# Kernel optimization log

Measured on AMD Instinct MI355X. Metric: run time of the kernel, lower is better.

The kernel has to match this reference:

```python
import jax, jax.numpy as jnp
import numpy as np

N_NODES = 50000
N_EDGES = 800000
D_IN = 64   # input_dimension + 1
D_HID = 64


def _gcn_conv(x, src, dst, W, b, deg_isqrt):
    # PyG GCNConv: X' = D^{-1/2} (A + I) D^{-1/2} X W + b
    h = x @ W  # [N, H]
    norm = (deg_isqrt[src] * deg_isqrt[dst])[:, None]  # [E, 1]
    agg = jax.ops.segment_sum(h[src] * norm, dst, num_segments=x.shape[0])
    # self-loop contribution: norm_ii = deg_isqrt[i]^2
    agg = agg + h * (deg_isqrt * deg_isqrt)[:, None]
    return agg + b


def setup_inputs() -> dict:
    key = jax.random.key(0)
    ks = jax.random.split(key, 8)
    x = jax.random.normal(ks[0], (N_NODES, D_IN), dtype=jnp.float32)
    edge_index = jax.random.randint(ks[1], (2, N_EDGES), 0, N_NODES, dtype=jnp.int32)
    s = 1.0 / np.sqrt(D_HID)
    W0 = jax.random.normal(ks[2], (D_IN, D_HID), dtype=jnp.float32) * s
    b0 = jnp.zeros((D_HID,), dtype=jnp.float32)
    W1 = jax.random.normal(ks[3], (D_HID, D_HID), dtype=jnp.float32) * s
    b1 = jnp.zeros((D_HID,), dtype=jnp.float32)
    W2 = jax.random.normal(ks[4], (D_HID, D_HID), dtype=jnp.float32) * s
    b2 = jnp.zeros((D_HID,), dtype=jnp.float32)
    Wout = jax.random.normal(ks[5], (D_HID, 1), dtype=jnp.float32) * s
    bout = jnp.zeros((1,), dtype=jnp.float32)
    return {"x": x, "edge_index": edge_index, "W0": W0, "b0": b0,
            "W1": W1, "b1": b1, "W2": W2, "b2": b2,
            "Wout": Wout, "bout": bout}


def reference(x, edge_index, W0, b0, W1, b1, W2, b2, Wout, bout):
    src, dst = edge_index[0], edge_index[1]
    n = x.shape[0]
    # degree with self-loop (edge weight 1.0 each)
    deg = jnp.zeros((n,), x.dtype).at[dst].add(1.0) + 1.0
    deg_isqrt = jax.lax.rsqrt(deg)
    h = jax.nn.relu(_gcn_conv(x, src, dst, W0, b0, deg_isqrt))
    h = jax.nn.relu(_gcn_conv(h, src, dst, W1, b1, deg_isqrt))
    h = jax.nn.relu(_gcn_conv(h, src, dst, W2, b2, deg_isqrt))
    return h @ Wout + bout  # [N, 1]
```

## Files before the change

### kernel.cpp

```cpp
#include <hip/hip_runtime.h>
#include <hip/hip_bf16.h>

#define D 64
#define N_NODES 50000
#define N_EDGES 800000
#define TILE 16

__global__ void hist_k(const int* __restrict__ dst, int* __restrict__ cnt, int E) {
    int i = blockIdx.x * blockDim.x + threadIdx.x;
    if (i < E) atomicAdd(&cnt[dst[i]], 1);
}

__global__ void scan1_k(const int* __restrict__ cnt, int* __restrict__ off,
                        int* __restrict__ bsum, float* __restrict__ dis, int N) {
    __shared__ int sh[256];
    int t = threadIdx.x;
    int i = blockIdx.x * 256 + t;
    int v = (i < N) ? cnt[i] : 0;
    sh[t] = v;
    __syncthreads();
#pragma unroll
    for (int d = 1; d < 256; d <<= 1) {
        int u = (t >= d) ? sh[t - d] : 0;
        __syncthreads();
        sh[t] += u;
        __syncthreads();
    }
    if (i < N) {
        off[i] = sh[t] - v;
        dis[i] = rsqrtf((float)v + 1.0f);
    }
    if (t == 255) bsum[blockIdx.x] = sh[255];
}

__global__ void scan2_k(int* __restrict__ bsum, int nb) {
    __shared__ int sh[256];
    int t = threadIdx.x;
    int v = (t < nb) ? bsum[t] : 0;
    sh[t] = v;
    __syncthreads();
#pragma unroll
    for (int d = 1; d < 256; d <<= 1) {
        int u = (t >= d) ? sh[t - d] : 0;
        __syncthreads();
        sh[t] += u;
        __syncthreads();
    }
    if (t < nb) bsum[t] = sh[t] - v;
}

__global__ void scan3_k(int* __restrict__ off, const int* __restrict__ bsum,
                        int* __restrict__ cursor, int N, int E) {
    int i = blockIdx.x * 256 + threadIdx.x;
    if (i < N) {
        int o = off[i] + bsum[blockIdx.x];
        off[i] = o;
        cursor[i] = o;
    }
    if (i == 0) off[N] = E;
}

__device__ __forceinline__ void fma4(float4& a, float s, float4 w) {
    a.x = fmaf(s, w.x, a.x);
    a.y = fmaf(s, w.y, a.y);
    a.z = fmaf(s, w.z, a.z);
    a.w = fmaf(s, w.w, a.w);
}

template <int SCALED>
__device__ __forceinline__ void tile_gemm(const float (*hbuf)[68], const float4* __restrict__ W4,
                                          const float* __restrict__ dis, float* __restrict__ outp,
                                          int base, int t) {
    int lane = t & 63;
    int cg = lane & 15;
    int rr = (t >> 6) * 4 + (lane >> 4);
    float4 acc = make_float4(0.f, 0.f, 0.f, 0.f);
#pragma unroll
    for (int kk = 0; kk < 16; ++kk) {
        float4 hb = *(const float4*)&hbuf[rr][kk * 4];
        fma4(acc, hb.x, W4[(kk * 4 + 0) * 16 + cg]);
        fma4(acc, hb.y, W4[(kk * 4 + 1) * 16 + cg]);
        fma4(acc, hb.z, W4[(kk * 4 + 2) * 16 + cg]);
        fma4(acc, hb.w, W4[(kk * 4 + 3) * 16 + cg]);
    }
    if (SCALED) {
        float dv = dis[base + rr];
        acc.x *= dv; acc.y *= dv; acc.z *= dv; acc.w *= dv;
    }
    ((float4*)outp)[(size_t)(base + rr) * 16 + cg] = acc;
}

__global__ void gemm0_k(const float4* __restrict__ X4, const float4* __restrict__ W4,
                        float* __restrict__ H, int N) {
    __shared__ float hbuf[TILE][68];
    int t = threadIdx.x;
    int base = blockIdx.x * TILE;
    int r = t >> 4, ch = t & 15;
    float4 v = X4[(size_t)(base + r) * 16 + ch];
    *(float4*)&hbuf[r][ch * 4] = v;
    __syncthreads();
    tile_gemm<0>(hbuf, W4, nullptr, H, base, t);
}

__global__ void fused_fill_k(const int* __restrict__ src, const int* __restrict__ dst,
                             int* __restrict__ cursor, int* __restrict__ esrc,
                             float4* __restrict__ H4, const float* __restrict__ dis,
                             int N, int E, int fillBlocks) {
    int bid = blockIdx.x;
    int t = threadIdx.x;
    if (bid < fillBlocks) {
        for (int i = bid * 256 + t; i < E; i += fillBlocks * 256) {
            int pos = atomicAdd(&cursor[dst[i]], 1);
            esrc[pos] = src[i];
        }
    } else {
        int sb = bid - fillBlocks;
        int nsb = gridDim.x - fillBlocks;
        int total = N * 16;
        for (int i = sb * 256 + t; i < total; i += nsb * 256) {
            float4 v = H4[i];
            float dv = dis[i >> 4];
            v.x *= dv; v.y *= dv; v.z *= dv; v.w *= dv;
            H4[i] = v;
        }
    }
}

template <int FINAL>
__global__ void layer_k(const float4* __restrict__ Hs4, const int* __restrict__ off,
                        const int* __restrict__ esrc, const float* __restrict__ dis,
                        const float* __restrict__ bias, const float4* __restrict__ W4,
                        const float* __restrict__ bout, float* __restrict__ outp, int N) {
    __shared__ float hbuf[TILE][68];
    int t = threadIdx.x;
    int lane = t & 63;
    int w = t >> 6;
    int g = lane >> 4;
    int l16 = lane & 15;
    int rloc = w * 4 + g;
    int n = blockIdx.x * TILE + rloc;

    int beg = off[n], end = off[n + 1];
    float4 acc = Hs4[(size_t)n * 16 + l16];
    int j = beg;
    for (; j + 8 <= end; j += 8) {
        int s0 = esrc[j],     s1 = esrc[j + 1], s2 = esrc[j + 2], s3 = esrc[j + 3];
        int s4 = esrc[j + 4], s5 = esrc[j + 5], s6 = esrc[j + 6], s7 = esrc[j + 7];
        float4 v0 = Hs4[(size_t)s0 * 16 + l16];
        float4 v1 = Hs4[(size_t)s1 * 16 + l16];
        float4 v2 = Hs4[(size_t)s2 * 16 + l16];
        float4 v3 = Hs4[(size_t)s3 * 16 + l16];
        float4 v4 = Hs4[(size_t)s4 * 16 + l16];
        float4 v5 = Hs4[(size_t)s5 * 16 + l16];
        float4 v6 = Hs4[(size_t)s6 * 16 + l16];
        float4 v7 = Hs4[(size_t)s7 * 16 + l16];
        acc.x += ((v0.x + v1.x) + (v2.x + v3.x)) + ((v4.x + v5.x) + (v6.x + v7.x));
        acc.y += ((v0.y + v1.y) + (v2.y + v3.y)) + ((v4.y + v5.y) + (v6.y + v7.y));
        acc.z += ((v0.z + v1.z) + (v2.z + v3.z)) + ((v4.z + v5.z) + (v6.z + v7.z));
        acc.w += ((v0.w + v1.w) + (v2.w + v3.w)) + ((v4.w + v5.w) + (v6.w + v7.w));
    }
    if (j < end) {
        int last = end - 1;
        int i1 = j + 1 <= last ? j + 1 : last;
        int i2 = j + 2 <= last ? j + 2 : last;
        int i3 = j + 3 <= last ? j + 3 : last;
        int i4 = j + 4 <= last ? j + 4 : last;
        int i5 = j + 5 <= last ? j + 5 : last;
        int i6 = j + 6 <= last ? j + 6 : last;
        int i7 = j + 7 <= last ? j + 7 : last;
        int s0 = esrc[j],  s1 = esrc[i1], s2 = esrc[i2], s3 = esrc[i3];
        int s4 = esrc[i4], s5 = esrc[i5], s6 = esrc[i6], s7 = esrc[i7];
        float m1 = (j + 1 < end) ? 1.f : 0.f;
        float m2 = (j + 2 < end) ? 1.f : 0.f;
        float m3 = (j + 3 < end) ? 1.f : 0.f;
        float m4 = (j + 4 < end) ? 1.f : 0.f;
        float m5 = (j + 5 < end) ? 1.f : 0.f;
        float m6 = (j + 6 < end) ? 1.f : 0.f;
        float m7 = (j + 7 < end) ? 1.f : 0.f;
        float4 v0 = Hs4[(size_t)s0 * 16 + l16];
        float4 v1 = Hs4[(size_t)s1 * 16 + l16];
        float4 v2 = Hs4[(size_t)s2 * 16 + l16];
        float4 v3 = Hs4[(size_t)s3 * 16 + l16];
        float4 v4 = Hs4[(size_t)s4 * 16 + l16];
        float4 v5 = Hs4[(size_t)s5 * 16 + l16];
        float4 v6 = Hs4[(size_t)s6 * 16 + l16];
        float4 v7 = Hs4[(size_t)s7 * 16 + l16];
        acc.x += v0.x;           acc.y += v0.y;           acc.z += v0.z;           acc.w += v0.w;
        acc.x = fmaf(m1, v1.x, acc.x); acc.y = fmaf(m1, v1.y, acc.y); acc.z = fmaf(m1, v1.z, acc.z); acc.w = fmaf(m1, v1.w, acc.w);
        acc.x = fmaf(m2, v2.x, acc.x); acc.y = fmaf(m2, v2.y, acc.y); acc.z = fmaf(m2, v2.z, acc.z); acc.w = fmaf(m2, v2.w, acc.w);
        acc.x = fmaf(m3, v3.x, acc.x); acc.y = fmaf(m3, v3.y, acc.y); acc.z = fmaf(m3, v3.z, acc.z); acc.w = fmaf(m3, v3.w, acc.w);
        acc.x = fmaf(m4, v4.x, acc.x); acc.y = fmaf(m4, v4.y, acc.y); acc.z = fmaf(m4, v4.z, acc.z); acc.w = fmaf(m4, v4.w, acc.w);
        acc.x = fmaf(m5, v5.x, acc.x); acc.y = fmaf(m5, v5.y, acc.y); acc.z = fmaf(m5, v5.z, acc.z); acc.w = fmaf(m5, v5.w, acc.w);
        acc.x = fmaf(m6, v6.x, acc.x); acc.y = fmaf(m6, v6.y, acc.y); acc.z = fmaf(m6, v6.z, acc.z); acc.w = fmaf(m6, v6.w, acc.w);
        acc.x = fmaf(m7, v7.x, acc.x); acc.y = fmaf(m7, v7.y, acc.y); acc.z = fmaf(m7, v7.z, acc.z); acc.w = fmaf(m7, v7.w, acc.w);
    }

    float dv = dis[n];
    float4 b4 = ((const float4*)bias)[l16];
    float4 h4;
    h4.x = fmaxf(fmaf(acc.x, dv, b4.x), 0.f);
    h4.y = fmaxf(fmaf(acc.y, dv, b4.y), 0.f);
    h4.z = fmaxf(fmaf(acc.z, dv, b4.z), 0.f);
    h4.w = fmaxf(fmaf(acc.w, dv, b4.w), 0.f);

    if (FINAL) {
        float4 w4 = ((const float4*)W4)[l16];
        float p = fmaf(h4.x, w4.x, fmaf(h4.y, w4.y, fmaf(h4.z, w4.z, h4.w * w4.w)));
        p += __shfl_xor(p, 1, 64);
        p += __shfl_xor(p, 2, 64);
        p += __shfl_xor(p, 4, 64);
        p += __shfl_xor(p, 8, 64);
        if (l16 == 0) outp[n] = p + bout[0];
    } else {
        *(float4*)&hbuf[rloc][l16 * 4] = h4;
        __syncthreads();
        tile_gemm<1>(hbuf, W4, dis, outp, blockIdx.x * TILE, t);
    }
}

extern "C" void kernel_launch(void* const* d_in, const int* in_sizes, int n_in,
                              void* d_out, int out_size, void* d_ws, size_t ws_size,
                              hipStream_t stream) {
    const float* x    = (const float*)d_in[0];
    const int*   ei   = (const int*)d_in[1];
    const float* W0   = (const float*)d_in[2];
    const float* b0   = (const float*)d_in[3];
    const float* W1   = (const float*)d_in[4];
    const float* b1   = (const float*)d_in[5];
    const float* W2   = (const float*)d_in[6];
    const float* b2   = (const float*)d_in[7];
    const float* Wout = (const float*)d_in[8];
    const float* bout = (const float*)d_in[9];
    float* out = (float*)d_out;

    const int N = N_NODES, E = N_EDGES;
    const int* src = ei;
    const int* dst = ei + E;

    char* ws = (char*)d_ws;
    int*   cnt    = (int*)(ws);
    int*   off    = (int*)(ws + (256u << 10));
    int*   cursor = (int*)(ws + (512u << 10));
    float* dis    = (float*)(ws + (768u << 10));
    int*   bsum   = (int*)(ws + (990u << 10));
    int*   esrc   = (int*)(ws + (1u << 20));
    float* bufA   = (float*)(ws + (5u << 20));
    float* bufB   = (float*)(ws + (18u << 20));

    dim3 blk(256);
    const int NB = (N + 255) / 256;
    dim3 gN(NB);
    dim3 gE((E + 255) / 256);
    const int TILES = N / TILE;
    dim3 gTile(TILES);
    const int FILL_BLOCKS = 3125;
    const int SCALE_BLOCKS = 784;

    hipMemsetAsync(cnt, 0, (size_t)N * sizeof(int), stream);
    hist_k<<<gE, blk, 0, stream>>>(dst, cnt, E);
    gemm0_k<<<gTile, blk, 0, stream>>>((const float4*)x, (const float4*)W0, bufA, N);

    scan1_k<<<gN, blk, 0, stream>>>(cnt, off, bsum, dis, N);
    scan2_k<<<1, blk, 0, stream>>>(bsum, NB);
    scan3_k<<<gN, blk, 0, stream>>>(off, bsum, cursor, N, E);

    fused_fill_k<<<dim3(FILL_BLOCKS + SCALE_BLOCKS), blk, 0, stream>>>(
        src, dst, cursor, esrc, (float4*)bufA, dis, N, E, FILL_BLOCKS);

    layer_k<0><<<gTile, blk, 0, stream>>>((const float4*)bufA, off, esrc, dis,
                                          b0, (const float4*)W1, nullptr, bufB, N);
    layer_k<0><<<gTile, blk, 0, stream>>>((const float4*)bufB, off, esrc, dis,
                                          b1, (const float4*)W2, nullptr, bufA, N);
    layer_k<1><<<gTile, blk, 0, stream>>>((const float4*)bufA, off, esrc, dis,
                                          b2, (const float4*)Wout, bout, out, N);
}
```

Before: 307.4 us.

## Fuse scan with first GEMM, merge scan stages, process two nodes per thread group

Merges the first scan pass with the initial dense GEMM into one launch and folds the block-sum scan into the final scan kernel, where every block rescans the block sums itself. This removes two kernel launches. The layer kernels now handle 32 nodes per block, with each 16-lane group aggregating two nodes in an interleaved loop so more independent gathers are in flight, and the tile GEMM reuses each loaded weight for two rows. In exchange the grid is halved, which may lower occupancy, and load imbalance between the paired nodes' degrees can leave lanes idle.

```diff
diff --git a/kernel.cpp b/kernel.cpp
--- a/kernel.cpp
+++ b/kernel.cpp
@@ -4,36 +4,96 @@
 #define D 64
 #define N_NODES 50000
 #define N_EDGES 800000
-#define TILE 16
+#define TILE 32
+#define SCAN_BLKS 196
 
 __global__ void hist_k(const int* __restrict__ dst, int* __restrict__ cnt, int E) {
     int i = blockIdx.x * blockDim.x + threadIdx.x;
     if (i < E) atomicAdd(&cnt[dst[i]], 1);
 }
 
-__global__ void scan1_k(const int* __restrict__ cnt, int* __restrict__ off,
-                        int* __restrict__ bsum, float* __restrict__ dis, int N) {
-    __shared__ int sh[256];
+__device__ __forceinline__ void fma4(float4& a, float s, float4 w) {
+    a.x = fmaf(s, w.x, a.x);
+    a.y = fmaf(s, w.y, a.y);
+    a.z = fmaf(s, w.z, a.z);
+    a.w = fmaf(s, w.w, a.w);
+}
+
+template <int SCALED>
+__device__ __forceinline__ void tile_gemm32(const float (*hbuf)[68], const float4* __restrict__ W4,
+                                            const float* __restrict__ dis, float* __restrict__ outp,
+                                            int base, int t, int N) {
+    int lane = t & 63;
+    int cg = lane & 15;
+    int rr = (t >> 6) * 4 + (lane >> 4);
+    int r1 = rr + 16;
+    float4 a0 = make_float4(0.f, 0.f, 0.f, 0.f);
+    float4 a1 = make_float4(0.f, 0.f, 0.f, 0.f);
+#pragma unroll
+    for (int kk = 0; kk < 16; ++kk) {
+        float4 h0 = *(const float4*)&hbuf[rr][kk * 4];
+        float4 h1 = *(const float4*)&hbuf[r1][kk * 4];
+        float4 w0 = W4[(kk * 4 + 0) * 16 + cg];
+        float4 w1 = W4[(kk * 4 + 1) * 16 + cg];
+        float4 w2 = W4[(kk * 4 + 2) * 16 + cg];
+        float4 w3 = W4[(kk * 4 + 3) * 16 + cg];
+        fma4(a0, h0.x, w0); fma4(a0, h0.y, w1); fma4(a0, h0.z, w2); fma4(a0, h0.w, w3);
+        fma4(a1, h1.x, w0); fma4(a1, h1.y, w1); fma4(a1, h1.z, w2); fma4(a1, h1.w, w3);
+    }
+    if (SCALED) {
+        float d0 = dis[base + rr];
+        a0.x *= d0; a0.y *= d0; a0.z *= d0; a0.w *= d0;
+    }
+    ((float4*)outp)[(size_t)(base + rr) * 16 + cg] = a0;
+    if (base + r1 < N) {
+        if (SCALED) {
+            float d1 = dis[base + r1];
+            a1.x *= d1; a1.y *= d1; a1.z *= d1; a1.w *= d1;
+        }
+        ((float4*)outp)[(size_t)(base + r1) * 16 + cg] = a1;
+    }
+}
+
+__global__ void scan1_gemm0_k(const int* __restrict__ cnt, int* __restrict__ off,
+                              int* __restrict__ bsum, float* __restrict__ dis,
+                              const float4* __restrict__ X4, const float4* __restrict__ W4,
+                              float* __restrict__ H, int N, int scanBlocks) {
+    __shared__ float hbuf[TILE][68];
+    int bid = blockIdx.x;
     int t = threadIdx.x;
-    int i = blockIdx.x * 256 + t;
-    int v = (i < N) ? cnt[i] : 0;
-    sh[t] = v;
-    __syncthreads();
+    if (bid < scanBlocks) {
+        int* sh = (int*)hbuf;
+        int i = bid * 256 + t;
+        int v = (i < N) ? cnt[i] : 0;
+        sh[t] = v;
+        __syncthreads();
 #pragma unroll
-    for (int d = 1; d < 256; d <<= 1) {
-        int u = (t >= d) ? sh[t - d] : 0;
-        __syncthreads();
-        sh[t] += u;
-        __syncthreads();
-    }
-    if (i < N) {
-        off[i] = sh[t] - v;
-        dis[i] = rsqrtf((float)v + 1.0f);
-    }
-    if (t == 255) bsum[blockIdx.x] = sh[255];
-}
-
-__global__ void scan2_k(int* __restrict__ bsum, int nb) {
+        for (int d = 1; d < 256; d <<= 1) {
+            int u = (t >= d) ? sh[t - d] : 0;
+            __syncthreads();
+            sh[t] += u;
+            __syncthreads();
+        }
+        if (i < N) {
+            off[i] = sh[t] - v;
+            dis[i] = rsqrtf((float)v + 1.0f);
+        }
+        if (t == 255) bsum[bid] = sh[255];
+    } else {
+        int base = (bid - scanBlocks) * TILE;
+        for (int idx = t; idx < TILE * 16; idx += 256) {
+            int r = idx >> 4, ch = idx & 15;
+            float4 v = (base + r < N) ? X4[(size_t)(base + r) * 16 + ch]
+                                      : make_float4(0.f, 0.f, 0.f, 0.f);
+            *(float4*)&hbuf[r][ch * 4] = v;
+        }
+        __syncthreads();
+        tile_gemm32<0>(hbuf, W4, nullptr, H, base, t, N);
+    }
+}
+
+__global__ void scan3_k(int* __restrict__ off, const int* __restrict__ bsum,
+                        int* __restrict__ cursor, int N, int E, int nb) {
     __shared__ int sh[256];
     int t = threadIdx.x;
     int v = (t < nb) ? bsum[t] : 0;
@@ -46,60 +106,14 @@
         sh[t] += u;
         __syncthreads();
     }
-    if (t < nb) bsum[t] = sh[t] - v;
-}
-
-__global__ void scan3_k(int* __restrict__ off, const int* __restrict__ bsum,
-                        int* __restrict__ cursor, int N, int E) {
-    int i = blockIdx.x * 256 + threadIdx.x;
+    int add = (blockIdx.x == 0) ? 0 : sh[blockIdx.x - 1];
+    int i = blockIdx.x * 256 + t;
     if (i < N) {
-        int o = off[i] + bsum[blockIdx.x];
+        int o = off[i] + add;
         off[i] = o;
         cursor[i] = o;
     }
     if (i == 0) off[N] = E;
-}
-
-__device__ __forceinline__ void fma4(float4& a, float s, float4 w) {
-    a.x = fmaf(s, w.x, a.x);
-    a.y = fmaf(s, w.y, a.y);
-    a.z = fmaf(s, w.z, a.z);
-    a.w = fmaf(s, w.w, a.w);
-}
-
-template <int SCALED>
-__device__ __forceinline__ void tile_gemm(const float (*hbuf)[68], const float4* __restrict__ W4,
-                                          const float* __restrict__ dis, float* __restrict__ outp,
-                                          int base, int t) {
-    int lane = t & 63;
-    int cg = lane & 15;
-    int rr = (t >> 6) * 4 + (lane >> 4);
-    float4 acc = make_float4(0.f, 0.f, 0.f, 0.f);
-#pragma unroll
-    for (int kk = 0; kk < 16; ++kk) {
-        float4 hb = *(const float4*)&hbuf[rr][kk * 4];
-        fma4(acc, hb.x, W4[(kk * 4 + 0) * 16 + cg]);
-        fma4(acc, hb.y, W4[(kk * 4 + 1) * 16 + cg]);
-        fma4(acc, hb.z, W4[(kk * 4 + 2) * 16 + cg]);
-        fma4(acc, hb.w, W4[(kk * 4 + 3) * 16 + cg]);
-    }
-    if (SCALED) {
-        float dv = dis[base + rr];
-        acc.x *= dv; acc.y *= dv; acc.z *= dv; acc.w *= dv;
-    }
-    ((float4*)outp)[(size_t)(base + rr) * 16 + cg] = acc;
-}
-
-__global__ void gemm0_k(const float4* __restrict__ X4, const float4* __restrict__ W4,
-                        float* __restrict__ H, int N) {
-    __shared__ float hbuf[TILE][68];
-    int t = threadIdx.x;
-    int base = blockIdx.x * TILE;
-    int r = t >> 4, ch = t & 15;
-    float4 v = X4[(size_t)(base + r) * 16 + ch];
-    *(float4*)&hbuf[r][ch * 4] = v;
-    __syncthreads();
-    tile_gemm<0>(hbuf, W4, nullptr, H, base, t);
 }
 
 __global__ void fused_fill_k(const int* __restrict__ src, const int* __restrict__ dst,
@@ -126,95 +140,132 @@
     }
 }
 
+__device__ __forceinline__ void batch8(const float4* __restrict__ Hs4,
+                                       const int* __restrict__ esrc,
+                                       int j, int l16, float4& acc) {
+    int s0 = esrc[j],     s1 = esrc[j + 1], s2 = esrc[j + 2], s3 = esrc[j + 3];
+    int s4 = esrc[j + 4], s5 = esrc[j + 5], s6 = esrc[j + 6], s7 = esrc[j + 7];
+    float4 v0 = Hs4[(size_t)s0 * 16 + l16];
+    float4 v1 = Hs4[(size_t)s1 * 16 + l16];
+    float4 v2 = Hs4[(size_t)s2 * 16 + l16];
+    float4 v3 = Hs4[(size_t)s3 * 16 + l16];
+    float4 v4 = Hs4[(size_t)s4 * 16 + l16];
+    float4 v5 = Hs4[(size_t)s5 * 16 + l16];
+    float4 v6 = Hs4[(size_t)s6 * 16 + l16];
+    float4 v7 = Hs4[(size_t)s7 * 16 + l16];
+    acc.x += ((v0.x + v1.x) + (v2.x + v3.x)) + ((v4.x + v5.x) + (v6.x + v7.x));
+    acc.y += ((v0.y + v1.y) + (v2.y + v3.y)) + ((v4.y + v5.y) + (v6.y + v7.y));
+    acc.z += ((v0.z + v1.z) + (v2.z + v3.z)) + ((v4.z + v5.z) + (v6.z + v7.z));
+    acc.w += ((v0.w + v1.w) + (v2.w + v3.w)) + ((v4.w + v5.w) + (v6.w + v7.w));
+}
+
+__device__ __forceinline__ void tail8(const float4* __restrict__ Hs4,
+                                      const int* __restrict__ esrc,
+                                      int j, int end, int l16, float4& acc) {
+    if (j >= end) return;
+    int last = end - 1;
+    int i1 = j + 1 <= last ? j + 1 : last;
+    int i2 = j + 2 <= last ? j + 2 : last;
+    int i3 = j + 3 <= last ? j + 3 : last;
+    int i4 = j + 4 <= last ? j + 4 : last;
+    int i5 = j + 5 <= last ? j + 5 : last;
+    int i6 = j + 6 <= last ? j + 6 : last;
+    int i7 = j + 7 <= last ? j + 7 : last;
+    int s0 = esrc[j],  s1 = esrc[i1], s2 = esrc[i2], s3 = esrc[i3];
+    int s4 = esrc[i4], s5 = esrc[i5], s6 = esrc[i6], s7 = esrc[i7];
+    float m1 = (j + 1 < end) ? 1.f : 0.f;
+    float m2 = (j + 2 < end) ? 1.f : 0.f;
+    float m3 = (j + 3 < end) ? 1.f : 0.f;
+    float m4 = (j + 4 < end) ? 1.f : 0.f;
+    float m5 = (j + 5 < end) ? 1.f : 0.f;
+    float m6 = (j + 6 < end) ? 1.f : 0.f;
+    float m7 = (j + 7 < end) ? 1.f : 0.f;
+    float4 v0 = Hs4[(size_t)s0 * 16 + l16];
+    float4 v1 = Hs4[(size_t)s1 * 16 + l16];
+    float4 v2 = Hs4[(size_t)s2 * 16 + l16];
+    float4 v3 = Hs4[(size_t)s3 * 16 + l16];
+    float4 v4 = Hs4[(size_t)s4 * 16 + l16];
+    float4 v5 = Hs4[(size_t)s5 * 16 + l16];
+    float4 v6 = Hs4[(size_t)s6 * 16 + l16];
+    float4 v7 = Hs4[(size_t)s7 * 16 + l16];
+    acc.x += v0.x; acc.y += v0.y; acc.z += v0.z; acc.w += v0.w;
+    acc.x = fmaf(m1, v1.x, acc.x); acc.y = fmaf(m1, v1.y, acc.y); acc.z = fmaf(m1, v1.z, acc.z); acc.w = fmaf(m1, v1.w, acc.w);
+    acc.x = fmaf(m2, v2.x, acc.x); acc.y = fmaf(m2, v2.y, acc.y); acc.z = fmaf(m2, v2.z, acc.z); acc.w = fmaf(m2, v2.w, acc.w);
+    acc.x = fmaf(m3, v3.x, acc.x); acc.y = fmaf(m3, v3.y, acc.y); acc.z = fmaf(m3, v3.z, acc.z); acc.w = fmaf(m3, v3.w, acc.w);
+    acc.x = fmaf(m4, v4.x, acc.x); acc.y = fmaf(m4, v4.y, acc.y); acc.z = fmaf(m4, v4.z, acc.z); acc.w = fmaf(m4, v4.w, acc.w);
+    acc.x = fmaf(m5, v5.x, acc.x); acc.y = fmaf(m5, v5.y, acc.y); acc.z = fmaf(m5, v5.z, acc.z); acc.w = fmaf(m5, v5.w, acc.w);
+    acc.x = fmaf(m6, v6.x, acc.x); acc.y = fmaf(m6, v6.y, acc.y); acc.z = fmaf(m6, v6.z, acc.z); acc.w = fmaf(m6, v6.w, acc.w);
+    acc.x = fmaf(m7, v7.x, acc.x); acc.y = fmaf(m7, v7.y, acc.y); acc.z = fmaf(m7, v7.z, acc.z); acc.w = fmaf(m7, v7.w, acc.w);
+}
+
 template <int FINAL>
 __global__ void layer_k(const float4* __restrict__ Hs4, const int* __restrict__ off,
                         const int* __restrict__ esrc, const float* __restrict__ dis,
                         const float* __restrict__ bias, const float4* __restrict__ W4,
                         const float* __restrict__ bout, float* __restrict__ outp, int N) {
-    __shared__ float hbuf[TILE][68];
     int t = threadIdx.x;
     int lane = t & 63;
     int w = t >> 6;
     int g = lane >> 4;
     int l16 = lane & 15;
     int rloc = w * 4 + g;
-    int n = blockIdx.x * TILE + rloc;
-
-    int beg = off[n], end = off[n + 1];
-    float4 acc = Hs4[(size_t)n * 16 + l16];
-    int j = beg;
-    for (; j + 8 <= end; j += 8) {
-        int s0 = esrc[j],     s1 = esrc[j + 1], s2 = esrc[j + 2], s3 = esrc[j + 3];
-        int s4 = esrc[j + 4], s5 = esrc[j + 5], s6 = esrc[j + 6], s7 = esrc[j + 7];
-        float4 v0 = Hs4[(size_t)s0 * 16 + l16];
-        float4 v1 = Hs4[(size_t)s1 * 16 + l16];
-        float4 v2 = Hs4[(size_t)s2 * 16 + l16];
-        float4 v3 = Hs4[(size_t)s3 * 16 + l16];
-        float4 v4 = Hs4[(size_t)s4 * 16 + l16];
-        float4 v5 = Hs4[(size_t)s5 * 16 + l16];
-        float4 v6 = Hs4[(size_t)s6 * 16 + l16];
-        float4 v7 = Hs4[(size_t)s7 * 16 + l16];
-        acc.x += ((v0.x + v1.x) + (v2.x + v3.x)) + ((v4.x + v5.x) + (v6.x + v7.x));
-        acc.y += ((v0.y + v1.y) + (v2.y + v3.y)) + ((v4.y + v5.y) + (v6.y + v7.y));
-        acc.z += ((v0.z + v1.z) + (v2.z + v3.z)) + ((v4.z + v5.z) + (v6.z + v7.z));
-        acc.w += ((v0.w + v1.w) + (v2.w + v3.w)) + ((v4.w + v5.w) + (v6.w + v7.w));
-    }
-    if (j < end) {
-        int last = end - 1;
-        int i1 = j + 1 <= last ? j + 1 : last;
-        int i2 = j + 2 <= last ? j + 2 : last;
-        int i3 = j + 3 <= last ? j + 3 : last;
-        int i4 = j + 4 <= last ? j + 4 : last;
-        int i5 = j + 5 <= last ? j + 5 : last;
-        int i6 = j + 6 <= last ? j + 6 : last;
-        int i7 = j + 7 <= last ? j + 7 : last;
-        int s0 = esrc[j],  s1 = esrc[i1], s2 = esrc[i2], s3 = esrc[i3];
-        int s4 = esrc[i4], s5 = esrc[i5], s6 = esrc[i6], s7 = esrc[i7];
-        float m1 = (j + 1 < end) ? 1.f : 0.f;
-        float m2 = (j + 2 < end) ? 1.f : 0.f;
-        float m3 = (j + 3 < end) ? 1.f : 0.f;
-        float m4 = (j + 4 < end) ? 1.f : 0.f;
-        float m5 = (j + 5 < end) ? 1.f : 0.f;
-        float m6 = (j + 6 < end) ? 1.f : 0.f;
-        float m7 = (j + 7 < end) ? 1.f : 0.f;
-        float4 v0 = Hs4[(size_t)s0 * 16 + l16];
-        float4 v1 = Hs4[(size_t)s1 * 16 + l16];
-        float4 v2 = Hs4[(size_t)s2 * 16 + l16];
-        float4 v3 = Hs4[(size_t)s3 * 16 + l16];
-        float4 v4 = Hs4[(size_t)s4 * 16 + l16];
-        float4 v5 = Hs4[(size_t)s5 * 16 + l16];
-        float4 v6 = Hs4[(size_t)s6 * 16 + l16];
-        float4 v7 = Hs4[(size_t)s7 * 16 + l16];
-        acc.x += v0.x;           acc.y += v0.y;           acc.z += v0.z;           acc.w += v0.w;
-        acc.x = fmaf(m1, v1.x, acc.x); acc.y = fmaf(m1, v1.y, acc.y); acc.z = fmaf(m1, v1.z, acc.z); acc.w = fmaf(m1, v1.w, acc.w);
-        acc.x = fmaf(m2, v2.x, acc.x); acc.y = fmaf(m2, v2.y, acc.y); acc.z = fmaf(m2, v2.z, acc.z); acc.w = fmaf(m2, v2.w, acc.w);
-        acc.x = fmaf(m3, v3.x, acc.x); acc.y = fmaf(m3, v3.y, acc.y); acc.z = fmaf(m3, v3.z, acc.z); acc.w = fmaf(m3, v3.w, acc.w);
-        acc.x = fmaf(m4, v4.x, acc.x); acc.y = fmaf(m4, v4.y, acc.y); acc.z = fmaf(m4, v4.z, acc.z); acc.w = fmaf(m4, v4.w, acc.w);
-        acc.x = fmaf(m5, v5.x, acc.x); acc.y = fmaf(m5, v5.y, acc.y); acc.z = fmaf(m5, v5.z, acc.z); acc.w = fmaf(m5, v5.w, acc.w);
-        acc.x = fmaf(m6, v6.x, acc.x); acc.y = fmaf(m6, v6.y, acc.y); acc.z = fmaf(m6, v6.z, acc.z); acc.w = fmaf(m6, v6.w, acc.w);
-        acc.x = fmaf(m7, v7.x, acc.x); acc.y = fmaf(m7, v7.y, acc.y); acc.z = fmaf(m7, v7.z, acc.z); acc.w = fmaf(m7, v7.w, acc.w);
-    }
-
-    float dv = dis[n];
+    int base = blockIdx.x * TILE;
+    int nA = base + rloc;
+    int nB = nA + 16;
+    bool vB = (nB < N);
+
+    int begA = off[nA], endA = off[nA + 1];
+    float4 accA = Hs4[(size_t)nA * 16 + l16];
+    int begB = 0, endB = 0;
+    float4 accB = make_float4(0.f, 0.f, 0.f, 0.f);
+    if (vB) {
+        begB = off[nB]; endB = off[nB + 1];
+        accB = Hs4[(size_t)nB * 16 + l16];
+    }
+
+    int jA = begA, jB = begB;
+    while (jA + 8 <= endA && jB + 8 <= endB) {
+        batch8(Hs4, esrc, jA, l16, accA);
+        batch8(Hs4, esrc, jB, l16, accB);
+        jA += 8; jB += 8;
+    }
+    while (jA + 8 <= endA) { batch8(Hs4, esrc, jA, l16, accA); jA += 8; }
+    while (jB + 8 <= endB) { batch8(Hs4, esrc, jB, l16, accB); jB += 8; }
+    tail8(Hs4, esrc, jA, endA, l16, accA);
+    tail8(Hs4, esrc, jB, endB, l16, accB);
+
+    float dvA = dis[nA];
+    float dvB = vB ? dis[nB] : 0.f;
     float4 b4 = ((const float4*)bias)[l16];
-    float4 h4;
-    h4.x = fmaxf(fmaf(acc.x, dv, b4.x), 0.f);
-    h4.y = fmaxf(fmaf(acc.y, dv, b4.y), 0.f);
-    h4.z = fmaxf(fmaf(acc.z, dv, b4.z), 0.f);
-    h4.w = fmaxf(fmaf(acc.w, dv, b4.w), 0.f);
+    float4 hA, hB;
+    hA.x = fmaxf(fmaf(accA.x, dvA, b4.x), 0.f);
+    hA.y = fmaxf(fmaf(accA.y, dvA, b4.y), 0.f);
+    hA.z = fmaxf(fmaf(accA.z, dvA, b4.z), 0.f);
+    hA.w = fmaxf(fmaf(accA.w, dvA, b4.w), 0.f);
+    hB.x = fmaxf(fmaf(accB.x, dvB, b4.x), 0.f);
+    hB.y = fmaxf(fmaf(accB.y, dvB, b4.y), 0.f);
+    hB.z = fmaxf(fmaf(accB.z, dvB, b4.z), 0.f);
+    hB.w = fmaxf(fmaf(accB.w, dvB, b4.w), 0.f);
 
     if (FINAL) {
         float4 w4 = ((const float4*)W4)[l16];
-        float p = fmaf(h4.x, w4.x, fmaf(h4.y, w4.y, fmaf(h4.z, w4.z, h4.w * w4.w)));
-        p += __shfl_xor(p, 1, 64);
-        p += __shfl_xor(p, 2, 64);
-        p += __shfl_xor(p, 4, 64);
-        p += __shfl_xor(p, 8, 64);
-        if (l16 == 0) outp[n] = p + bout[0];
+        float pA = fmaf(hA.x, w4.x, fmaf(hA.y, w4.y, fmaf(hA.z, w4.z, hA.w * w4.w)));
+        float pB = fmaf(hB.x, w4.x, fmaf(hB.y, w4.y, fmaf(hB.z, w4.z, hB.w * w4.w)));
+        pA += __shfl_xor(pA, 1, 64);  pB += __shfl_xor(pB, 1, 64);
+        pA += __shfl_xor(pA, 2, 64);  pB += __shfl_xor(pB, 2, 64);
+        pA += __shfl_xor(pA, 4, 64);  pB += __shfl_xor(pB, 4, 64);
+        pA += __shfl_xor(pA, 8, 64);  pB += __shfl_xor(pB, 8, 64);
+        if (l16 == 0) {
+            float b = bout[0];
+            outp[nA] = pA + b;
+            if (vB) outp[nB] = pB + b;
+        }
     } else {
-        *(float4*)&hbuf[rloc][l16 * 4] = h4;
-        __syncthreads();
-        tile_gemm<1>(hbuf, W4, dis, outp, blockIdx.x * TILE, t);
+        __shared__ float hbuf[TILE][68];
+        *(float4*)&hbuf[rloc][l16 * 4] = hA;
+        *(float4*)&hbuf[rloc + 16][l16 * 4] = hB;
+        __syncthreads();
+        tile_gemm32<1>(hbuf, W4, dis, outp, base, t, N);
     }
 }
 
@@ -248,21 +299,19 @@
     float* bufB   = (float*)(ws + (18u << 20));
 
     dim3 blk(256);
-    const int NB = (N + 255) / 256;
-    dim3 gN(NB);
     dim3 gE((E + 255) / 256);
-    const int TILES = N / TILE;
+    const int TILES = (N + TILE - 1) / TILE;
     dim3 gTile(TILES);
     const int FILL_BLOCKS = 3125;
     const int SCALE_BLOCKS = 784;
 
     hipMemsetAsync(cnt, 0, (size_t)N * sizeof(int), stream);
     hist_k<<<gE, blk, 0, stream>>>(dst, cnt, E);
-    gemm0_k<<<gTile, blk, 0, stream>>>((const float4*)x, (const float4*)W0, bufA, N);
-
-    scan1_k<<<gN, blk, 0, stream>>>(cnt, off, bsum, dis, N);
-    scan2_k<<<1, blk, 0, stream>>>(bsum, NB);
-    scan3_k<<<gN, blk, 0, stream>>>(off, bsum, cursor, N, E);
+
+    scan1_gemm0_k<<<dim3(SCAN_BLKS + TILES), blk, 0, stream>>>(
+        cnt, off, bsum, dis, (const float4*)x, (const float4*)W0, bufA, N, SCAN_BLKS);
+
+    scan3_k<<<dim3(SCAN_BLKS), blk, 0, stream>>>(off, bsum, cursor, N, E, SCAN_BLKS);
 
     fused_fill_k<<<dim3(FILL_BLOCKS + SCALE_BLOCKS), blk, 0, stream>>>(
         src, dst, cursor, esrc, (float4*)bufA, dis, N, E, FILL_BLOCKS);
```

After: 553.8 us. 80.2% more time.

## Fuse scan phase one with first GEMM and fold block-sum scan into scan3

Applied to the files above, without the earlier changes.

Merges the first scan pass and the layer-0 feature GEMM into one heterogeneous launch, where some blocks scan degree counts and the rest compute X@W0. The GEMM now works on 32-row tiles so each W load serves two rows. The separate block-sum scan kernel is removed; every scan3 block rescans the 196 block sums itself. Together this removes two kernel launches and their serialization gaps. The cost is redundant scan work in each scan3 block and more register pressure in the GEMM path.

```diff
diff --git a/kernel.cpp b/kernel.cpp
--- a/kernel.cpp
+++ b/kernel.cpp
@@ -5,59 +5,12 @@
 #define N_NODES 50000
 #define N_EDGES 800000
 #define TILE 16
+#define GTILE 32
+#define SCAN_BLKS 196
 
 __global__ void hist_k(const int* __restrict__ dst, int* __restrict__ cnt, int E) {
     int i = blockIdx.x * blockDim.x + threadIdx.x;
     if (i < E) atomicAdd(&cnt[dst[i]], 1);
-}
-
-__global__ void scan1_k(const int* __restrict__ cnt, int* __restrict__ off,
-                        int* __restrict__ bsum, float* __restrict__ dis, int N) {
-    __shared__ int sh[256];
-    int t = threadIdx.x;
-    int i = blockIdx.x * 256 + t;
-    int v = (i < N) ? cnt[i] : 0;
-    sh[t] = v;
-    __syncthreads();
-#pragma unroll
-    for (int d = 1; d < 256; d <<= 1) {
-        int u = (t >= d) ? sh[t - d] : 0;
-        __syncthreads();
-        sh[t] += u;
-        __syncthreads();
-    }
-    if (i < N) {
-        off[i] = sh[t] - v;
-        dis[i] = rsqrtf((float)v + 1.0f);
-    }
-    if (t == 255) bsum[blockIdx.x] = sh[255];
-}
-
-__global__ void scan2_k(int* __restrict__ bsum, int nb) {
-    __shared__ int sh[256];
-    int t = threadIdx.x;
-    int v = (t < nb) ? bsum[t] : 0;
-    sh[t] = v;
-    __syncthreads();
-#pragma unroll
-    for (int d = 1; d < 256; d <<= 1) {
-        int u = (t >= d) ? sh[t - d] : 0;
-        __syncthreads();
-        sh[t] += u;
-        __syncthreads();
-    }
-    if (t < nb) bsum[t] = sh[t] - v;
-}
-
-__global__ void scan3_k(int* __restrict__ off, const int* __restrict__ bsum,
-                        int* __restrict__ cursor, int N, int E) {
-    int i = blockIdx.x * 256 + threadIdx.x;
-    if (i < N) {
-        int o = off[i] + bsum[blockIdx.x];
-        off[i] = o;
-        cursor[i] = o;
-    }
-    if (i == 0) off[N] = E;
 }
 
 __device__ __forceinline__ void fma4(float4& a, float s, float4 w) {
@@ -90,16 +43,90 @@
     ((float4*)outp)[(size_t)(base + rr) * 16 + cg] = acc;
 }
 
-__global__ void gemm0_k(const float4* __restrict__ X4, const float4* __restrict__ W4,
-                        float* __restrict__ H, int N) {
-    __shared__ float hbuf[TILE][68];
+__device__ __forceinline__ void tile_gemm32(const float (*hbuf)[68], const float4* __restrict__ W4,
+                                            float* __restrict__ outp, int base, int t, int N) {
+    int lane = t & 63;
+    int cg = lane & 15;
+    int rr = (t >> 6) * 4 + (lane >> 4);
+    int r1 = rr + 16;
+    float4 a0 = make_float4(0.f, 0.f, 0.f, 0.f);
+    float4 a1 = make_float4(0.f, 0.f, 0.f, 0.f);
+#pragma unroll
+    for (int kk = 0; kk < 16; ++kk) {
+        float4 h0 = *(const float4*)&hbuf[rr][kk * 4];
+        float4 h1 = *(const float4*)&hbuf[r1][kk * 4];
+        float4 w0 = W4[(kk * 4 + 0) * 16 + cg];
+        float4 w1 = W4[(kk * 4 + 1) * 16 + cg];
+        float4 w2 = W4[(kk * 4 + 2) * 16 + cg];
+        float4 w3 = W4[(kk * 4 + 3) * 16 + cg];
+        fma4(a0, h0.x, w0); fma4(a0, h0.y, w1); fma4(a0, h0.z, w2); fma4(a0, h0.w, w3);
+        fma4(a1, h1.x, w0); fma4(a1, h1.y, w1); fma4(a1, h1.z, w2); fma4(a1, h1.w, w3);
+    }
+    ((float4*)outp)[(size_t)(base + rr) * 16 + cg] = a0;
+    if (base + r1 < N)
+        ((float4*)outp)[(size_t)(base + r1) * 16 + cg] = a1;
+}
+
+__global__ void scan1_gemm0_k(const int* __restrict__ cnt, int* __restrict__ off,
+                              int* __restrict__ bsum, float* __restrict__ dis,
+                              const float4* __restrict__ X4, const float4* __restrict__ W4,
+                              float* __restrict__ H, int N, int scanBlocks) {
+    __shared__ float hbuf[GTILE][68];
+    int bid = blockIdx.x;
     int t = threadIdx.x;
-    int base = blockIdx.x * TILE;
-    int r = t >> 4, ch = t & 15;
-    float4 v = X4[(size_t)(base + r) * 16 + ch];
-    *(float4*)&hbuf[r][ch * 4] = v;
+    if (bid < scanBlocks) {
+        int* sh = (int*)hbuf;
+        int i = bid * 256 + t;
+        int v = (i < N) ? cnt[i] : 0;
+        sh[t] = v;
+        __syncthreads();
+#pragma unroll
+        for (int d = 1; d < 256; d <<= 1) {
+            int u = (t >= d) ? sh[t - d] : 0;
+            __syncthreads();
+            sh[t] += u;
+            __syncthreads();
+        }
+        if (i < N) {
+            off[i] = sh[t] - v;
+            dis[i] = rsqrtf((float)v + 1.0f);
+        }
+        if (t == 255) bsum[bid] = sh[255];
+    } else {
+        int base = (bid - scanBlocks) * GTILE;
+        for (int idx = t; idx < GTILE * 16; idx += 256) {
+            int r = idx >> 4, ch = idx & 15;
+            float4 v = (base + r < N) ? X4[(size_t)(base + r) * 16 + ch]
+                                      : make_float4(0.f, 0.f, 0.f, 0.f);
+            *(float4*)&hbuf[r][ch * 4] = v;
+        }
+        __syncthreads();
+        tile_gemm32(hbuf, W4, H, base, t, N);
+    }
+}
+
+__global__ void scan3_k(int* __restrict__ off, const int* __restrict__ bsum,
+                        int* __restrict__ cursor, int N, int E, int nb) {
+    __shared__ int sh[256];
+    int t = threadIdx.x;
+    int v = (t < nb) ? bsum[t] : 0;
+    sh[t] = v;
     __syncthreads();
-    tile_gemm<0>(hbuf, W4, nullptr, H, base, t);
+#pragma unroll
+    for (int d = 1; d < 256; d <<= 1) {
+        int u = (t >= d) ? sh[t - d] : 0;
+        __syncthreads();
+        sh[t] += u;
+        __syncthreads();
+    }
+    int add = (blockIdx.x == 0) ? 0 : sh[blockIdx.x - 1];
+    int i = blockIdx.x * 256 + t;
+    if (i < N) {
+        int o = off[i] + add;
+        off[i] = o;
+        cursor[i] = o;
+    }
+    if (i == 0) off[N] = E;
 }
 
 __global__ void fused_fill_k(const int* __restrict__ src, const int* __restrict__ dst,
@@ -185,7 +212,7 @@
         float4 v5 = Hs4[(size_t)s5 * 16 + l16];
         float4 v6 = Hs4[(size_t)s6 * 16 + l16];
         float4 v7 = Hs4[(size_t)s7 * 16 + l16];
-        acc.x += v0.x;           acc.y += v0.y;           acc.z += v0.z;           acc.w += v0.w;
+        acc.x += v0.x; acc.y += v0.y; acc.z += v0.z; acc.w += v0.w;
         acc.x = fmaf(m1, v1.x, acc.x); acc.y = fmaf(m1, v1.y, acc.y); acc.z = fmaf(m1, v1.z, acc.z); acc.w = fmaf(m1, v1.w, acc.w);
         acc.x = fmaf(m2, v2.x, acc.x); acc.y = fmaf(m2, v2.y, acc.y); acc.z = fmaf(m2, v2.z, acc.z); acc.w = fmaf(m2, v2.w, acc.w);
         acc.x = fmaf(m3, v3.x, acc.x); acc.y = fmaf(m3, v3.y, acc.y); acc.z = fmaf(m3, v3.z, acc.z); acc.w = fmaf(m3, v3.w, acc.w);
@@ -248,29 +275,28 @@
     float* bufB   = (float*)(ws + (18u << 20));
 
     dim3 blk(256);
-    const int NB = (N + 255) / 256;
-    dim3 gN(NB);
     dim3 gE((E + 255) / 256);
-    const int TILES = N / TILE;
-    dim3 gTile(TILES);
+    const int LTILES = N / TILE;
+    dim3 gLayer(LTILES);
+    const int GTILES = (N + GTILE - 1) / GTILE;
     const int FILL_BLOCKS = 3125;
     const int SCALE_BLOCKS = 784;
 
     hipMemsetAsync(cnt, 0, (size_t)N * sizeof(int), stream);
     hist_k<<<gE, blk, 0, stream>>>(dst, cnt, E);
-    gemm0_k<<<gTile, blk, 0, stream>>>((const float4*)x, (const float4*)W0, bufA, N);
-
-    scan1_k<<<gN, blk, 0, stream>>>(cnt, off, bsum, dis, N);
-    scan2_k<<<1, blk, 0, stream>>>(bsum, NB);
-    scan3_k<<<gN, blk, 0, stream>>>(off, bsum, cursor, N, E);
+
+    scan1_gemm0_k<<<dim3(SCAN_BLKS + GTILES), blk, 0, stream>>>(
+        cnt, off, bsum, dis, (const float4*)x, (const float4*)W0, bufA, N, SCAN_BLKS);
+
+    scan3_k<<<dim3(SCAN_BLKS), blk, 0, stream>>>(off, bsum, cursor, N, E, SCAN_BLKS);
 
     fused_fill_k<<<dim3(FILL_BLOCKS + SCALE_BLOCKS), blk, 0, stream>>>(
         src, dst, cursor, esrc, (float4*)bufA, dis, N, E, FILL_BLOCKS);
 
-    layer_k<0><<<gTile, blk, 0, stream>>>((const float4*)bufA, off, esrc, dis,
-                                          b0, (const float4*)W1, nullptr, bufB, N);
-    layer_k<0><<<gTile, blk, 0, stream>>>((const float4*)bufB, off, esrc, dis,
-                                          b1, (const float4*)W2, nullptr, bufA, N);
-    layer_k<1><<<gTile, blk, 0, stream>>>((const float4*)bufA, off, esrc, dis,
-                                          b2, (const float4*)Wout, bout, out, N);
-}
+    layer_k<0><<<gLayer, blk, 0, stream>>>((const float4*)bufA, off, esrc, dis,
+                                           b0, (const float4*)W1, nullptr, bufB, N);
+    layer_k<0><<<gLayer, blk, 0, stream>>>((const float4*)bufB, off, esrc, dis,
+                                           b1, (const float4*)W2, nullptr, bufA, N);
+    layer_k<1><<<gLayer, blk, 0, stream>>>((const float4*)bufA, off, esrc, dis,
+                                           b2, (const float4*)Wout, bout, out, N);
+}
```

Result: slower. 376.3 us (+22.4%).
